# Optimization experiments

Measured on AMD Instinct MI355X. Metric: run time of the kernel, lower is better.

The kernel has to match this reference:

```python
import jax, jax.numpy as jnp
import numpy as np
import math

SH_DEGREE = 8
FULL_BASIS = False


def _even_indices_and_number(sh_degree, full_basis):
    if full_basis:
        number = (sh_degree + 1) * (sh_degree + 1)
        n_range = np.arange(0, sh_degree + 1, dtype=int)
    else:
        number = (sh_degree + 1) * (sh_degree + 2) // 2
        n_range = np.arange(0, sh_degree + 1, 2, dtype=int)
    n_list = np.repeat(n_range, n_range * 2 + 1)
    even = np.where(n_list % 2 == 0)[0]
    return even, number


def construct_filter(f, sh_degree=SH_DEGREE, full_basis=FULL_BASIS):
    # f: [in_channel, S, L] -> [1, in_channel, S, C]
    L = f.shape[2]
    scale = np.array([math.sqrt(4 * math.pi / (4 * l + 1)) for l in range(L)], np.float32)
    f = f * scale[None, None, :]
    # repeat_interleave with repeats 4l+1 expressed as a static gather
    rep_idx = np.repeat(np.arange(L), [4 * l + 1 for l in range(L)])
    f = f[:, :, rep_idx]  # [ch, S, sum(4l+1)]
    even, number = _even_indices_and_number(sh_degree, full_basis)
    full = jnp.zeros((1, f.shape[0], f.shape[1], number), f.dtype)
    full = full.at[..., even].set(f[None])
    return full


def setup_inputs() -> dict:
    key = jax.random.key(0)
    k1, k2, k3, k4, k5 = jax.random.split(key, 5)
    B, CH_E, CH_I, C, S, Vs, X = 1, 2, 2, 45, 3, 64, 48
    return {
        "x_equi_shc": jax.random.normal(k1, (B, CH_E, C, X, X, X), jnp.float32),
        "x_inva_shc": jax.random.normal(k2, (B, CH_I, 1, X, X, X), jnp.float32),
        "polar_filter_equi": jax.random.normal(k3, (CH_E, S, 5), jnp.float32),
        "polar_filter_inva": jax.random.normal(k4, (CH_I, S, 1), jnp.float32),
        "Y": jax.random.normal(k5, (S, Vs, C), jnp.float32),  # per-shell SH basis
    }


def reference(x_equi_shc, x_inva_shc, polar_filter_equi, polar_filter_inva, Y):
    B = x_equi_shc.shape[0]
    S, Vs, C = Y.shape
    X1, X2, X3 = x_equi_shc.shape[-3:]

    # --- equivariant branch ---
    fe = construct_filter(polar_filter_equi)  # [1, ch, S, C]
    # IsoSHConv: broadcast multiply -> [B, ch, S, C, X, Y, Z]
    x_equi_conv_shc = x_equi_shc[:, :, None] * fe[..., None, None, None]
    # ShellComputeSignal (per-shell basis contraction) + channel sum
    sig_equi = jnp.einsum("svc,bnscxyz->bsvxyz", Y, x_equi_conv_shc)
    sig_equi = sig_equi.reshape(B, S * Vs, X1, X2, X3)

    # --- invariant branch (C_in = 1; filter nonzero only at coeff 0) ---
    fi = construct_filter(polar_filter_inva)  # [1, ch, S, C]
    xi = x_inva_shc[:, :, 0]  # [B, ch, X, Y, Z]
    sig_inva = jnp.einsum("svc,nsc,bnxyz->bsvxyz", Y, fi[0], xi)
    sig_inva = sig_inva.reshape(B, S * Vs, X1, X2, X3)

    x_reconstructed = sig_equi + sig_inva
    return (x_reconstructed, x_equi_conv_shc)
```

## Files before the change

### kernel.cpp

```cpp
#include <hip/hip_runtime.h>
#include <math.h>

typedef float f2 __attribute__((ext_vector_type(2)));
typedef float f4 __attribute__((ext_vector_type(4)));

#define NP 110592
#define OUT1_OFF (192 * NP)

__global__ __launch_bounds__(256, 2) void recon_kernel(
    const float* __restrict__ xe,
    const float* __restrict__ xiv,
    const float* __restrict__ pfe,
    const float* __restrict__ pfi,
    const float* __restrict__ Y,
    float* __restrict__ out)
{
    __shared__ __align__(16) float Yp[64 * 48];
    __shared__ float feS[90];
    __shared__ float gS[2];

    const int tid = threadIdx.x;
    const int bid = blockIdx.x;
    const int s   = bid % 3;
    const int vb  = bid / 3;

    for (int i = tid; i < 64 * 45; i += 256) {
        int row = i / 45;
        int c   = i - row * 45;
        Yp[row * 48 + c] = Y[(s * 64 + row) * 45 + c];
    }
    if (tid < 128) {
        int row = tid >> 1;
        Yp[row * 48 + 46 + (tid & 1)] = 0.f;
    }
    if (tid < 90) {
        int n = tid / 45;
        int c = tid - n * 45;
        int l = (c == 0) ? 0 : (c < 6) ? 1 : (c < 15) ? 2 : (c < 28) ? 3 : 4;
        feS[tid] = pfe[(n * 3 + s) * 5 + l] * sqrtf(4.f * (float)M_PI / (float)(4 * l + 1));
    }
    if (tid < 2) gS[tid] = pfi[tid * 3 + s] * sqrtf(4.f * (float)M_PI);
    __syncthreads();
    if (tid < 64) {
        float sum = 0.f;
        #pragma unroll
        for (int c = 0; c < 45; ++c) sum += Yp[tid * 48 + c];
        Yp[tid * 48 + 45] = sum;
    }
    __syncthreads();

    const int p0 = (vb * 256 + tid) * 2;

    f2 tt[48];

    const float* xep = xe + p0;
    float* o1 = out + OUT1_OFF + (size_t)s * 45 * NP + p0;

    #pragma unroll
    for (int c = 0; c < 45; ++c) {
        f2 x0 = *(const f2*)(xep + (size_t)c * NP);
        f2 x1 = *(const f2*)(xep + (size_t)(45 + c) * NP);
        float f0 = feS[c], f1 = feS[45 + c];
        f2 v0 = f0 * x0;
        f2 v1 = f1 * x1;
        __builtin_nontemporal_store(v0, (f2*)(o1 + (size_t)c * NP));
        __builtin_nontemporal_store(v1, (f2*)(o1 + (size_t)(135 + c) * NP));
        tt[c] = v0 + v1;
    }
    {
        f2 a0 = *(const f2*)(xiv + p0);
        f2 a1 = *(const f2*)(xiv + NP + p0);
        f2 u  = gS[0] * a0 + gS[1] * a1;
        tt[45] = u;
        f2 z = {0.f, 0.f};
        tt[46] = z;
        tt[47] = z;
    }

    float* o0 = out + (size_t)s * 64 * NP + p0;
    #pragma unroll 2
    for (int v = 0; v < 64; ++v) {
        const f4* yr = (const f4*)&Yp[v * 48];
        f2 accA = {0.f, 0.f}, accB = {0.f, 0.f};
        #pragma unroll
        for (int j = 0; j < 12; j += 2) {
            f4 ya = yr[j];
            f4 yb = yr[j + 1];
            accA += ya.x * tt[4 * j + 0];
            accA += ya.y * tt[4 * j + 1];
            accA += ya.z * tt[4 * j + 2];
            accA += ya.w * tt[4 * j + 3];
            accB += yb.x * tt[4 * j + 4];
            accB += yb.y * tt[4 * j + 5];
            accB += yb.z * tt[4 * j + 6];
            accB += yb.w * tt[4 * j + 7];
        }
        f2 acc = accA + accB;
        __builtin_nontemporal_store(acc, (f2*)(o0 + (size_t)v * NP));
    }
}

extern "C" void kernel_launch(void* const* d_in, const int* in_sizes, int n_in,
                              void* d_out, int out_size, void* d_ws, size_t ws_size,
                              hipStream_t stream) {
    const float* xe  = (const float*)d_in[0];
    const float* xiv = (const float*)d_in[1];
    const float* pfe = (const float*)d_in[2];
    const float* pfi = (const float*)d_in[3];
    const float* Y   = (const float*)d_in[4];
    float* out = (float*)d_out;
    (void)in_sizes; (void)n_in; (void)d_ws; (void)ws_size; (void)out_size;

    recon_kernel<<<dim3(648), dim3(256), 0, stream>>>(xe, xiv, pfe, pfi, Y, out);
}
```

Measured before the change: 268.2 us.

## Process four points per thread with 64-thread blocks and float4 accesses

Each thread now handles four spatial points instead of two, using float4 loads and nontemporal stores, and blocks shrink to a single 64-thread wavefront across twice as many blocks. Each Y-row sum is computed straight from global memory during setup, which removes one barrier, and the zero-padding terms in the contraction are dropped. This widens memory transactions and amortizes each shared Y read over more outputs. In exchange it roughly doubles per-thread registers (46 float4 values held live), which risks spilling or lower occupancy, and each block now redoes the Y staging for only 64 threads.

Result: no change. 268.5 us (+0.1%).

```diff
diff --git a/kernel.cpp b/kernel.cpp
--- a/kernel.cpp
+++ b/kernel.cpp
@@ -7,7 +7,7 @@
 #define NP 110592
 #define OUT1_OFF (192 * NP)
 
-__global__ __launch_bounds__(256, 2) void recon_kernel(
+__global__ __launch_bounds__(64, 2) void recon_kernel(
     const float* __restrict__ xe,
     const float* __restrict__ xiv,
     const float* __restrict__ pfe,
@@ -24,66 +24,57 @@
     const int s   = bid % 3;
     const int vb  = bid / 3;
 
-    for (int i = tid; i < 64 * 45; i += 256) {
+    for (int i = tid; i < 64 * 45; i += 64) {
         int row = i / 45;
         int c   = i - row * 45;
         Yp[row * 48 + c] = Y[(s * 64 + row) * 45 + c];
     }
-    if (tid < 128) {
-        int row = tid >> 1;
-        Yp[row * 48 + 46 + (tid & 1)] = 0.f;
+    {
+        const float* yrow = Y + (s * 64 + tid) * 45;
+        float sum = 0.f;
+        #pragma unroll
+        for (int c = 0; c < 45; ++c) sum += yrow[c];
+        Yp[tid * 48 + 45] = sum;
     }
-    if (tid < 90) {
-        int n = tid / 45;
-        int c = tid - n * 45;
+    for (int i = tid; i < 90; i += 64) {
+        int n = i / 45;
+        int c = i - n * 45;
         int l = (c == 0) ? 0 : (c < 6) ? 1 : (c < 15) ? 2 : (c < 28) ? 3 : 4;
-        feS[tid] = pfe[(n * 3 + s) * 5 + l] * sqrtf(4.f * (float)M_PI / (float)(4 * l + 1));
+        feS[i] = pfe[(n * 3 + s) * 5 + l] * sqrtf(4.f * (float)M_PI / (float)(4 * l + 1));
     }
     if (tid < 2) gS[tid] = pfi[tid * 3 + s] * sqrtf(4.f * (float)M_PI);
     __syncthreads();
-    if (tid < 64) {
-        float sum = 0.f;
-        #pragma unroll
-        for (int c = 0; c < 45; ++c) sum += Yp[tid * 48 + c];
-        Yp[tid * 48 + 45] = sum;
-    }
-    __syncthreads();
 
-    const int p0 = (vb * 256 + tid) * 2;
+    const int p0 = (vb * 64 + tid) * 4;
 
-    f2 tt[48];
+    f4 tt[46];
 
     const float* xep = xe + p0;
     float* o1 = out + OUT1_OFF + (size_t)s * 45 * NP + p0;
 
     #pragma unroll
     for (int c = 0; c < 45; ++c) {
-        f2 x0 = *(const f2*)(xep + (size_t)c * NP);
-        f2 x1 = *(const f2*)(xep + (size_t)(45 + c) * NP);
-        float f0 = feS[c], f1 = feS[45 + c];
-        f2 v0 = f0 * x0;
-        f2 v1 = f1 * x1;
-        __builtin_nontemporal_store(v0, (f2*)(o1 + (size_t)c * NP));
-        __builtin_nontemporal_store(v1, (f2*)(o1 + (size_t)(135 + c) * NP));
+        f4 x0 = *(const f4*)(xep + (size_t)c * NP);
+        f4 x1 = *(const f4*)(xep + (size_t)(45 + c) * NP);
+        f4 v0 = feS[c] * x0;
+        f4 v1 = feS[45 + c] * x1;
+        __builtin_nontemporal_store(v0, (f4*)(o1 + (size_t)c * NP));
+        __builtin_nontemporal_store(v1, (f4*)(o1 + (size_t)(135 + c) * NP));
         tt[c] = v0 + v1;
     }
     {
-        f2 a0 = *(const f2*)(xiv + p0);
-        f2 a1 = *(const f2*)(xiv + NP + p0);
-        f2 u  = gS[0] * a0 + gS[1] * a1;
-        tt[45] = u;
-        f2 z = {0.f, 0.f};
-        tt[46] = z;
-        tt[47] = z;
+        f4 a0 = *(const f4*)(xiv + p0);
+        f4 a1 = *(const f4*)(xiv + NP + p0);
+        tt[45] = gS[0] * a0 + gS[1] * a1;
     }
 
     float* o0 = out + (size_t)s * 64 * NP + p0;
     #pragma unroll 2
     for (int v = 0; v < 64; ++v) {
         const f4* yr = (const f4*)&Yp[v * 48];
-        f2 accA = {0.f, 0.f}, accB = {0.f, 0.f};
+        f4 accA = {0.f, 0.f, 0.f, 0.f}, accB = {0.f, 0.f, 0.f, 0.f};
         #pragma unroll
-        for (int j = 0; j < 12; j += 2) {
+        for (int j = 0; j < 10; j += 2) {
             f4 ya = yr[j];
             f4 yb = yr[j + 1];
             accA += ya.x * tt[4 * j + 0];
@@ -95,8 +86,20 @@
             accB += yb.z * tt[4 * j + 6];
             accB += yb.w * tt[4 * j + 7];
         }
-        f2 acc = accA + accB;
-        __builtin_nontemporal_store(acc, (f2*)(o0 + (size_t)v * NP));
+        {
+            f4 ya = yr[10];
+            accA += ya.x * tt[40];
+            accA += ya.y * tt[41];
+            accA += ya.z * tt[42];
+            accA += ya.w * tt[43];
+        }
+        {
+            f2 y2 = *(const f2*)&Yp[v * 48 + 44];
+            accB += y2.x * tt[44];
+            accB += y2.y * tt[45];
+        }
+        f4 acc = accA + accB;
+        __builtin_nontemporal_store(acc, (f4*)(o0 + (size_t)v * NP));
     }
 }
 
@@ -111,5 +114,5 @@
     float* out = (float*)d_out;
     (void)in_sizes; (void)n_in; (void)d_ws; (void)ws_size; (void)out_size;
 
-    recon_kernel<<<dim3(648), dim3(256), 0, stream>>>(xe, xiv, pfe, pfi, Y, out);
+    recon_kernel<<<dim3(1296), dim3(64), 0, stream>>>(xe, xiv, pfe, pfi, Y, out);
 }
```
